# Optimization experiments

Measured on AMD Instinct MI355X. Metric: run time of the kernel, lower is better.

## Reference

```python
import jax, jax.numpy as jnp
import numpy as np

B, F, T, L = 65536, 512, 8, 4


def setup_inputs() -> dict:
    key = jax.random.key(0)
    k1, k2, k3, k4, k5 = jax.random.split(key, 5)
    scale = 1.0 / np.sqrt(F)  # keep the 4-deep cross stack numerically tame
    return {
        "x": jax.random.normal(k1, (B, F), dtype=jnp.float32),
        "cross_w": jax.random.normal(k2, (L, F), dtype=jnp.float32) * scale,
        "cross_b": jax.random.normal(k3, (L, F), dtype=jnp.float32) * 0.1,
        "W_out": jax.random.normal(k4, (F, T), dtype=jnp.float32) * scale,
        "b_out": jax.random.normal(k5, (T,), dtype=jnp.float32) * 0.1,
    }


def reference(x, cross_w, cross_b, W_out, b_out):
    # DCN cross layers. torch does bmm(x0[:, :, None], x[:, None, :]) -> [B,F,F]
    # then tensordot with weights over the last axis; algebraically identical to
    # x0 * (x . w), which we compute directly (no O(B*F*F) intermediate).
    x0 = x
    for i in range(L):  # small fixed layer loop
        s = jnp.einsum("bf,f->b", x, cross_w[i])  # [B]
        x = x0 * s[:, None] + cross_b[i] + x
    return x @ W_out + b_out  # final Linear [B, T]
```

## Files before the change

### kernel.cpp

```cpp
#include <hip/hip_runtime.h>
#include <hip/hip_bf16.h>


typedef float v4f __attribute__((ext_vector_type(4)));
typedef float f32x4 __attribute__((ext_vector_type(4)));
typedef short s16x8 __attribute__((ext_vector_type(8)));

__device__ __forceinline__ short f2bf(float v) {
  return __builtin_bit_cast(short, __float2bfloat16(v));
}
__device__ __forceinline__ float bf2f(short s) {
  return __uint_as_float(((unsigned)(unsigned short)s) << 16);
}

template<int CTRL>
__device__ __forceinline__ float dpp_add(float v) {
  int t = __builtin_amdgcn_update_dpp(0, __float_as_int(v), CTRL, 0xF, 0xF, true);
  return v + __int_as_float(t);
}
__device__ __forceinline__ float wave_reduce(float v) {
  v = dpp_add<0x111>(v); v = dpp_add<0x112>(v); v = dpp_add<0x114>(v);
  v = dpp_add<0x118>(v); v = dpp_add<0x142>(v); v = dpp_add<0x143>(v);
  return v;
}

__global__ __launch_bounds__(256, 8) void cross_occ(
    const float* __restrict__ x, const float* __restrict__ cw,
    const float* __restrict__ cb, const float* __restrict__ Wo,
    const float* __restrict__ bo, float* __restrict__ out)
{
  __shared__ s16x8 Bh[16][64];
  __shared__ float ct[2][16][17];
  __shared__ float egs[12];

  const int tid = threadIdx.x, lane = tid & 63, wv = tid >> 6;
  const int tile = wv >> 1;
  const int kh   = wv & 1;
  const int row0 = (blockIdx.x << 5) + (tile << 4);

  const float* xr = x + (size_t)(row0 + (lane & 15)) * 512 + (kh << 8)
                      + ((lane >> 4) << 3);

  v4f xa[3], xb[3];
  #pragma unroll
  for (int p = 0; p < 3; ++p) {
    xa[p] = *(const v4f*)(xr + p * 32);
    xb[p] = *(const v4f*)(xr + p * 32 + 4);
  }

  for (int slot = tid; slot < 1024; slot += 256) {
    const int s = slot >> 6, l = slot & 63;
    const int c = l & 15, k0 = s * 32 + ((l >> 4) << 3);
    float f[8];
    if (c < 4) {
      v4f a = *(const v4f*)(cw + c * 512 + k0);
      v4f b = *(const v4f*)(cw + c * 512 + k0 + 4);
      #pragma unroll
      for (int j = 0; j < 4; ++j) { f[j] = a[j]; f[4 + j] = b[j]; }
    } else if (c < 12) {
      #pragma unroll
      for (int j = 0; j < 8; ++j) f[j] = Wo[(k0 + j) * 8 + (c - 4)];
    } else {
      #pragma unroll
      for (int j = 0; j < 8; ++j) f[j] = 0.f;
    }
    s16x8 h;
    #pragma unroll
    for (int j = 0; j < 8; ++j) h[j] = f2bf(f[j]);
    Bh[s][l] = h;
  }

  if (wv == 0) {
    const int f0 = lane << 3;
    float e1p = 0.f, e2p = 0.f, e3p = 0.f;
    v4f dA = *(const v4f*)(cb + f0), dB = *(const v4f*)(cb + f0 + 4);
    {
      v4f wa = *(const v4f*)(cw + 512 + f0), wb = *(const v4f*)(cw + 512 + f0 + 4);
      #pragma unroll
      for (int e = 0; e < 4; ++e) e1p += dA[e] * wa[e] + dB[e] * wb[e];
    }
    dA += *(const v4f*)(cb + 512 + f0); dB += *(const v4f*)(cb + 512 + f0 + 4);
    {
      v4f wa = *(const v4f*)(cw + 1024 + f0), wb = *(const v4f*)(cw + 1024 + f0 + 4);
      #pragma unroll
      for (int e = 0; e < 4; ++e) e2p += dA[e] * wa[e] + dB[e] * wb[e];
    }
    dA += *(const v4f*)(cb + 1024 + f0); dB += *(const v4f*)(cb + 1024 + f0 + 4);
    {
      v4f wa = *(const v4f*)(cw + 1536 + f0), wb = *(const v4f*)(cw + 1536 + f0 + 4);
      #pragma unroll
      for (int e = 0; e < 4; ++e) e3p += dA[e] * wa[e] + dB[e] * wb[e];
    }
    dA += *(const v4f*)(cb + 1536 + f0); dB += *(const v4f*)(cb + 1536 + f0 + 4);
    float gp[8] = {0.f,0.f,0.f,0.f,0.f,0.f,0.f,0.f};
    #pragma unroll
    for (int e = 0; e < 4; ++e) {
      const float* wra = Wo + (f0 + e) * 8;
      const float* wrb = Wo + (f0 + 4 + e) * 8;
      #pragma unroll
      for (int t = 0; t < 8; ++t) gp[t] += dA[e] * wra[t] + dB[e] * wrb[t];
    }
    e1p = wave_reduce(e1p); e2p = wave_reduce(e2p); e3p = wave_reduce(e3p);
    #pragma unroll
    for (int t = 0; t < 8; ++t) gp[t] = wave_reduce(gp[t]);
    if (lane == 63) {
      egs[0] = e1p; egs[1] = e2p; egs[2] = e3p;
      #pragma unroll
      for (int t = 0; t < 8; ++t) egs[3 + t] = gp[t] + bo[t];
    }
  }
  __syncthreads();

  f32x4 acc = {0.f, 0.f, 0.f, 0.f};
  #pragma unroll
  for (int s = 0; s < 8; ++s) {
    const int cur = s % 3;
    const v4f pa = xa[cur], pb = xb[cur];
    if (s + 3 < 8) {
      xa[cur] = *(const v4f*)(xr + (s + 3) * 32);
      xb[cur] = *(const v4f*)(xr + (s + 3) * 32 + 4);
    }
    const s16x8 bh = Bh[(kh << 3) + s][lane];
    s16x8 ah, al;
    #pragma unroll
    for (int j = 0; j < 4; ++j) {
      ah[j]     = f2bf(pa[j]); al[j]     = f2bf(pa[j] - bf2f(ah[j]));
      ah[4 + j] = f2bf(pb[j]); al[4 + j] = f2bf(pb[j] - bf2f(ah[4 + j]));
    }
    acc = __builtin_amdgcn_mfma_f32_16x16x32_bf16(ah, bh, acc, 0, 0, 0);
    acc = __builtin_amdgcn_mfma_f32_16x16x32_bf16(al, bh, acc, 0, 0, 0);
  }

  if (kh == 0) {
    #pragma unroll
    for (int j = 0; j < 4; ++j)
      ct[tile][((lane >> 4) << 2) + j][lane & 15] = acc[j];
  }
  __syncthreads();
  if (kh == 1) {
    #pragma unroll
    for (int j = 0; j < 4; ++j)
      ct[tile][((lane >> 4) << 2) + j][lane & 15] += acc[j];
  }
  __syncthreads();

  if (kh == 0 && lane < 16) {
    const float e1 = egs[0], e2 = egs[1], e3 = egs[2];
    const float u0 = ct[tile][lane][0], u1 = ct[tile][lane][1];
    const float u2 = ct[tile][lane][2], u3 = ct[tile][lane][3];
    const float cc1 = 1.f + u0;
    const float cc2 = fmaf(cc1, u1, cc1) + e1;
    const float cc3 = fmaf(cc2, u2, cc2) + e2;
    const float cc4 = fmaf(cc3, u3, cc3) + e3;
    v4f o0, o1;
    #pragma unroll
    for (int t = 0; t < 4; ++t) {
      o0[t] = fmaf(cc4, ct[tile][lane][4 + t], egs[3 + t]);
      o1[t] = fmaf(cc4, ct[tile][lane][8 + t], egs[7 + t]);
    }
    float* op = out + (size_t)(row0 + lane) * 8;
    *(v4f*)(op)     = o0;
    *(v4f*)(op + 4) = o1;
  }
}

extern "C" void kernel_launch(void* const* d_in, const int* in_sizes, int n_in,
                              void* d_out, int out_size, void* d_ws, size_t ws_size,
                              hipStream_t stream) {
  const float* x  = (const float*)d_in[0];
  const float* cw = (const float*)d_in[1];
  const float* cb = (const float*)d_in[2];
  const float* Wo = (const float*)d_in[3];
  const float* bo = (const float*)d_in[4];
  float* out = (float*)d_out;
  const int B = in_sizes[0] / 512;
  hipLaunchKernelGGL(cross_occ, dim3(B >> 5), dim3(256), 0, stream,
                     x, cw, cb, Wo, bo, out);
}
```

Measured before the change: 36.61 us.

## Give each wave full K range, drop cross-wave reduction, use nontemporal loads

Each wave now owns 16 rows and walks the full 512-wide feature dimension, so the block covers 64 rows instead of 32 and launches half as many blocks. This removes the two block barriers and the shared-memory merging of the two K-half partial sums. Loads of x become nontemporal so the streamed input does not pollute cache. The trade-off is a longer per-wave serial MFMA chain and a lower launch-bounds occupancy hint, with fewer blocks to hide memory latency. The barrier is replaced by a waitcnt on wave-private shared memory.

```diff
diff --git a/kernel.cpp b/kernel.cpp
--- a/kernel.cpp
+++ b/kernel.cpp
@@ -24,28 +24,24 @@
   return v;
 }
 
-__global__ __launch_bounds__(256, 8) void cross_occ(
+__global__ __launch_bounds__(256, 4) void cross_nt(
     const float* __restrict__ x, const float* __restrict__ cw,
     const float* __restrict__ cb, const float* __restrict__ Wo,
     const float* __restrict__ bo, float* __restrict__ out)
 {
   __shared__ s16x8 Bh[16][64];
-  __shared__ float ct[2][16][17];
+  __shared__ float ct[4][16][17];
   __shared__ float egs[12];
 
   const int tid = threadIdx.x, lane = tid & 63, wv = tid >> 6;
-  const int tile = wv >> 1;
-  const int kh   = wv & 1;
-  const int row0 = (blockIdx.x << 5) + (tile << 4);
-
-  const float* xr = x + (size_t)(row0 + (lane & 15)) * 512 + (kh << 8)
-                      + ((lane >> 4) << 3);
+  const int row0 = (blockIdx.x << 6) + (wv << 4);
+  const float* xr = x + (size_t)(row0 + (lane & 15)) * 512 + ((lane >> 4) << 3);
 
   v4f xa[3], xb[3];
   #pragma unroll
   for (int p = 0; p < 3; ++p) {
-    xa[p] = *(const v4f*)(xr + p * 32);
-    xb[p] = *(const v4f*)(xr + p * 32 + 4);
+    xa[p] = __builtin_nontemporal_load((const v4f*)(xr + p * 32));
+    xb[p] = __builtin_nontemporal_load((const v4f*)(xr + p * 32 + 4));
   }
 
   for (int slot = tid; slot < 1024; slot += 256) {
@@ -113,14 +109,14 @@
 
   f32x4 acc = {0.f, 0.f, 0.f, 0.f};
   #pragma unroll
-  for (int s = 0; s < 8; ++s) {
+  for (int s = 0; s < 16; ++s) {
     const int cur = s % 3;
     const v4f pa = xa[cur], pb = xb[cur];
-    if (s + 3 < 8) {
-      xa[cur] = *(const v4f*)(xr + (s + 3) * 32);
-      xb[cur] = *(const v4f*)(xr + (s + 3) * 32 + 4);
+    if (s + 3 < 16) {
+      xa[cur] = __builtin_nontemporal_load((const v4f*)(xr + (s + 3) * 32));
+      xb[cur] = __builtin_nontemporal_load((const v4f*)(xr + (s + 3) * 32 + 4));
     }
-    const s16x8 bh = Bh[(kh << 3) + s][lane];
+    const s16x8 bh = Bh[s][lane];
     s16x8 ah, al;
     #pragma unroll
     for (int j = 0; j < 4; ++j) {
@@ -131,23 +127,18 @@
     acc = __builtin_amdgcn_mfma_f32_16x16x32_bf16(al, bh, acc, 0, 0, 0);
   }
 
-  if (kh == 0) {
-    #pragma unroll
-    for (int j = 0; j < 4; ++j)
-      ct[tile][((lane >> 4) << 2) + j][lane & 15] = acc[j];
-  }
-  __syncthreads();
-  if (kh == 1) {
-    #pragma unroll
-    for (int j = 0; j < 4; ++j)
-      ct[tile][((lane >> 4) << 2) + j][lane & 15] += acc[j];
-  }
-  __syncthreads();
+  const float e1 = egs[0], e2 = egs[1], e3 = egs[2];
+  float gg[8];
+  #pragma unroll
+  for (int t = 0; t < 8; ++t) gg[t] = egs[3 + t];
 
-  if (kh == 0 && lane < 16) {
-    const float e1 = egs[0], e2 = egs[1], e3 = egs[2];
-    const float u0 = ct[tile][lane][0], u1 = ct[tile][lane][1];
-    const float u2 = ct[tile][lane][2], u3 = ct[tile][lane][3];
+  #pragma unroll
+  for (int j = 0; j < 4; ++j)
+    ct[wv][((lane >> 4) << 2) + j][lane & 15] = acc[j];
+  __builtin_amdgcn_s_waitcnt(0);
+  if (lane < 16) {
+    const float u0 = ct[wv][lane][0], u1 = ct[wv][lane][1];
+    const float u2 = ct[wv][lane][2], u3 = ct[wv][lane][3];
     const float cc1 = 1.f + u0;
     const float cc2 = fmaf(cc1, u1, cc1) + e1;
     const float cc3 = fmaf(cc2, u2, cc2) + e2;
@@ -155,8 +146,8 @@
     v4f o0, o1;
     #pragma unroll
     for (int t = 0; t < 4; ++t) {
-      o0[t] = fmaf(cc4, ct[tile][lane][4 + t], egs[3 + t]);
-      o1[t] = fmaf(cc4, ct[tile][lane][8 + t], egs[7 + t]);
+      o0[t] = fmaf(cc4, ct[wv][lane][4 + t], gg[t]);
+      o1[t] = fmaf(cc4, ct[wv][lane][8 + t], gg[4 + t]);
     }
     float* op = out + (size_t)(row0 + lane) * 8;
     *(v4f*)(op)     = o0;
@@ -174,6 +165,6 @@
   const float* bo = (const float*)d_in[4];
   float* out = (float*)d_out;
   const int B = in_sizes[0] / 512;
-  hipLaunchKernelGGL(cross_occ, dim3(B >> 5), dim3(256), 0, stream,
+  hipLaunchKernelGGL(cross_nt, dim3(B >> 6), dim3(256), 0, stream,
                      x, cw, cb, Wo, bo, out);
 }
```

Measured after the change: 34.98 us. -4.5%, faster.
